# Optimization experiments

Hardware: AMD Instinct MI355X
Metric: run time of the kernel (lower is better)

Reference implementation:

```python
import jax, jax.numpy as jnp
import numpy as np

N, E, D_IN, D_OUT, R, B = 50000, 800000, 100, 100, 200, 50
BN_EPS = 1e-5


def setup_inputs() -> dict:
    key = jax.random.key(0)
    ks = jax.random.split(key, 24)
    inv_in = 1.0 / np.sqrt(D_IN)
    lin = lambda k: (jax.random.uniform(k, (D_OUT, D_IN), jnp.float32, -inv_in, inv_in),
                     jax.random.uniform(jax.random.fold_in(k, 1), (D_OUT,), jnp.float32, -inv_in, inv_in))
    Ws_w, Ws_b = lin(ks[0])
    Wk_w, Wk_b = lin(ks[1])
    Wq_w, Wq_b = lin(ks[2])
    Wv_w, Wv_b = lin(ks[3])
    Wr_w, Wr_b = lin(ks[4])
    return {
        "n_in_feats": jax.random.normal(ks[5], (N, D_IN), jnp.float32),
        "r_feats": jax.random.normal(ks[6], (R, D_IN), jnp.float32),
        "src": jax.random.randint(ks[7], (E,), 0, N),
        "dst": jax.random.randint(ks[8], (E,), 0, N),
        "etype": jax.random.randint(ks[9], (E,), 0, R),
        "norm": jax.random.uniform(ks[10], (E, 1), jnp.float32),
        "Ws_w": Ws_w, "Ws_b": Ws_b,
        "Wk_w": Wk_w, "Wk_b": Wk_b,
        "Wq_w": Wq_w, "Wq_b": Wq_b,
        "Wv_w": Wv_w, "Wv_b": Wv_b,
        "Wr_w": Wr_w, "Wr_b": Wr_b,
        "relation_att": jax.random.normal(ks[11], (B, D_OUT), jnp.float32) * np.sqrt(2.0 / (B + D_OUT)),
        "w_comp": jax.random.normal(ks[12], (R, B), jnp.float32) * np.sqrt(2.0 / (R + B)),
        "alpha": jnp.ones((1,), jnp.float32),
        "loop_rel": jax.random.normal(ks[13], (1, D_IN), jnp.float32) * np.sqrt(2.0 / (1 + D_IN)),
        "bn_gamma": jnp.ones((D_OUT,), jnp.float32),
        "bn_beta": jnp.zeros((D_OUT,), jnp.float32),
    }


def reference(n_in_feats, r_feats, src, dst, etype, norm,
              Ws_w, Ws_b, Wk_w, Wk_b, Wq_w, Wq_b, Wv_w, Wv_b, Wr_w, Wr_b,
              relation_att, w_comp, alpha, loop_rel, bn_gamma, bn_beta):
    num_nodes = n_in_feats.shape[0]
    # relation features incl. self-loop relation (appended row)
    r_all = jnp.concatenate([r_feats, loop_rel], axis=0)          # [R+1, D_in]
    # basis-decomposed per-relation attention weights: [R, D_out]
    rel_w = jnp.matmul(w_comp, relation_att)
    # node projections, then gather per edge (edge_attention)
    k = jnp.matmul(n_in_feats, Wk_w.T) + Wk_b                     # [N, D_out]
    q = jnp.matmul(n_in_feats, Wq_w.T) + Wq_b
    v = jnp.matmul(n_in_feats, Wv_w.T) + Wv_b
    k_e = k[src]                                                   # [E, D_out]
    q_e = q[dst]
    v_e = v[src]
    w_e = rel_w[etype]                                             # [E, D_out]
    att = jnp.sum(k_e * w_e * q_e, axis=-1)                       # [E]
    # segment softmax over incoming edges of each dst node
    seg_max = jax.ops.segment_max(att, dst, num_segments=num_nodes)
    e = jnp.exp(att - seg_max[dst])
    denom = jax.ops.segment_sum(e, dst, num_segments=num_nodes)
    att_w = e / denom[dst]                                         # [E]
    final = jax.ops.segment_sum(att_w[:, None] * v_e, dst, num_segments=num_nodes)  # [N, D_out]
    # gated combination (dropout is identity in eval)
    a = jax.nn.sigmoid(alpha[0])
    n_out = a * (jnp.matmul(n_in_feats, Ws_w.T) + Ws_b) + (1.0 - a) * final
    # BatchNorm1d (training-mode batch stats, biased variance)
    mu = jnp.mean(n_out, axis=0)
    var = jnp.mean((n_out - mu) ** 2, axis=0)
    n_out = (n_out - mu) * jax.lax.rsqrt(var + BN_EPS) * bn_gamma + bn_beta
    n_out = jnp.tanh(n_out)
    r_out = jnp.matmul(r_all, Wr_w.T) + Wr_b                      # [R+1, D_out]
    return n_out, r_out[:-1]
```

## Files before the change

### kernel.cpp

```cpp
#include <hip/hip_runtime.h>
#include <hip/hip_bf16.h>
#include <math.h>

#define N_NODES 50000
#define N_EDGES 800000
#define BN_EPS  1e-5f
#define SCAN_NB 49
#define AGG_NB  2048

typedef float floatx2 __attribute__((ext_vector_type(2)));
typedef _Float16 half2_t __attribute__((ext_vector_type(2)));

#if defined(__has_builtin) && __has_builtin(__builtin_amdgcn_fdot2)
#define FDOT2(a, b, c) __builtin_amdgcn_fdot2((a), (b), (c), false)
#else
#define FDOT2(a, b, c) ((c) + (float)(a).x * (float)(b).x + (float)(a).y * (float)(b).y)
#endif

union h2u { half2_t h; unsigned u; };

#define OFS_RELW   0
#define OFS_KVP    25600
#define OFS_Q      3225600
#define OFS_BNPART 9625600
#define OFS_BNSC   10035200
#define OFS_BNSH   10035328
#define OFS_CNT    10035456
#define OFS_PART   10085632
#define OFS_BSUM   10135808
#define OFS_OFFS   10135872
#define OFS_RANK   10186048
#define OFS_PEDGE  10986048
#define OFS_WT     11786048
#define WS_ELEMS   11806848

__global__ __launch_bounds__(256) void prep_kernel(
    const float* __restrict__ wcomp, const float* __restrict__ ratt,
    const float* __restrict__ Wk, const float* __restrict__ Wq,
    const float* __restrict__ Wv, const float* __restrict__ Ws,
    float* __restrict__ relw, unsigned* __restrict__ Wth,
    int* __restrict__ cnt)
{
    const int b = blockIdx.x;
    const int tid = threadIdx.x;
    if (b < 196) {
        int i = b * 256 + tid;
        if (i < 50176) cnt[i] = 0;
    } else if (b < 296) {
        int o = (b - 196) * 256 + tid;
        if (o < 200 * 128) {
            int r = o / 128, c = o % 128;
            float acc = 0.f;
            if (c < 100) {
                #pragma unroll 10
                for (int k = 0; k < 50; ++k)
                    acc += wcomp[r * 50 + k] * ratt[k * 100 + c];
            }
            relw[o] = acc;
        }
    } else {
        int o = (b - 296) * 256 + tid;
        if (o < 4 * 50 * 104) {
            int m = o / 5200, rem = o % 5200, d2 = rem / 104, c = rem % 104;
            const float* W = (m == 0) ? Wk : (m == 1) ? Wq : (m == 2) ? Wv : Ws;
            float a = (c < 100) ? W[c * 100 + 2 * d2]     : 0.f;
            float bb = (c < 100) ? W[c * 100 + 2 * d2 + 1] : 0.f;
            h2u cv; cv.h = half2_t{(_Float16)a, (_Float16)bb};
            Wth[o] = cv.u;
        }
    }
}

__global__ __launch_bounds__(512) void proj_kernel(
    const float* __restrict__ X, const unsigned* __restrict__ Wth,
    const float* __restrict__ bk, const float* __restrict__ bq,
    const float* __restrict__ bv, const float* __restrict__ bs,
    unsigned* __restrict__ kvp, float* __restrict__ qo,
    float* __restrict__ so)
{
    __shared__ unsigned Xth[50][68];
    __shared__ unsigned Wlh[50][104];
    const int tid = threadIdx.x;
    const int nb  = blockIdx.x * 64;
    const int m   = blockIdx.y;

    const float* bp = (m == 0) ? bk : (m == 1) ? bq : (m == 2) ? bv : bs;

    for (int idx = tid; idx < 1300; idx += 512) {
        int r = idx / 26, c4 = idx % 26;
        uint4 w = ((const uint4*)(Wth + m * 5200 + r * 104))[c4];
        *(uint4*)&Wlh[r][c4 * 4] = w;
    }
    for (int idx = tid; idx < 1600; idx += 512) {
        int n = idx / 25, d4 = idx % 25;
        int node = nb + n;
        float4 x = (node < N_NODES)
                   ? ((const float4*)(X + (size_t)node * 100))[d4]
                   : make_float4(0.f, 0.f, 0.f, 0.f);
        const int col = n ^ ((d4 & 7) << 2);
        h2u c0, c1;
        c0.h = half2_t{(_Float16)x.x, (_Float16)x.y};
        c1.h = half2_t{(_Float16)x.z, (_Float16)x.w};
        Xth[2 * d4][col]     = c0.u;
        Xth[2 * d4 + 1][col] = c1.u;
    }
    __syncthreads();

    const int nt  = tid & 15;
    const int ct  = tid >> 4;
    const bool act = (ct < 25);
    const int cts  = act ? ct : 24;

    float acc[4][4];
    #pragma unroll
    for (int i = 0; i < 4; ++i)
        #pragma unroll
        for (int j = 0; j < 4; ++j) acc[i][j] = 0.f;

    #pragma unroll 5
    for (int d2 = 0; d2 < 50; ++d2) {
        const int key = ((d2 >> 1) & 7) << 2;
        const uint4 xv = *(const uint4*)&Xth[d2][(4 * nt) ^ key];
        const uint4 wv = *(const uint4*)&Wlh[d2][4 * cts];
        h2u x0, x1, x2, x3, w0, w1, w2, w3;
        x0.u = xv.x; x1.u = xv.y; x2.u = xv.z; x3.u = xv.w;
        w0.u = wv.x; w1.u = wv.y; w2.u = wv.z; w3.u = wv.w;
        acc[0][0] = FDOT2(x0.h, w0.h, acc[0][0]);
        acc[0][1] = FDOT2(x0.h, w1.h, acc[0][1]);
        acc[0][2] = FDOT2(x0.h, w2.h, acc[0][2]);
        acc[0][3] = FDOT2(x0.h, w3.h, acc[0][3]);
        acc[1][0] = FDOT2(x1.h, w0.h, acc[1][0]);
        acc[1][1] = FDOT2(x1.h, w1.h, acc[1][1]);
        acc[1][2] = FDOT2(x1.h, w2.h, acc[1][2]);
        acc[1][3] = FDOT2(x1.h, w3.h, acc[1][3]);
        acc[2][0] = FDOT2(x2.h, w0.h, acc[2][0]);
        acc[2][1] = FDOT2(x2.h, w1.h, acc[2][1]);
        acc[2][2] = FDOT2(x2.h, w2.h, acc[2][2]);
        acc[2][3] = FDOT2(x2.h, w3.h, acc[2][3]);
        acc[3][0] = FDOT2(x3.h, w0.h, acc[3][0]);
        acc[3][1] = FDOT2(x3.h, w1.h, acc[3][1]);
        acc[3][2] = FDOT2(x3.h, w2.h, acc[3][2]);
        acc[3][3] = FDOT2(x3.h, w3.h, acc[3][3]);
    }

    const float4 bb = act ? *(const float4*)(bp + ct * 4)
                          : make_float4(0.f, 0.f, 0.f, 0.f);
    if (m == 0 || m == 2) {
        const int wofs = (m == 0) ? ct : (32 + ct);
        #pragma unroll
        for (int i = 0; i < 4; ++i) {
            const int node = nb + nt * 4 + i;
            if (node < N_NODES) {
                unsigned wdo = 0u;
                if (act) {
                    int wd = 0;
                    wd = __builtin_amdgcn_cvt_pk_fp8_f32(
                        acc[i][0] + bb.x, acc[i][1] + bb.y, wd, false);
                    wd = __builtin_amdgcn_cvt_pk_fp8_f32(
                        acc[i][2] + bb.z, acc[i][3] + bb.w, wd, true);
                    wdo = (unsigned)wd;
                }
                kvp[(size_t)node * 64 + wofs] = wdo;
            }
        }
    } else if (m == 1) {
        #pragma unroll
        for (int i = 0; i < 4; ++i) {
            const int node = nb + nt * 4 + i;
            if (node < N_NODES) {
                float4 r = act ? make_float4(acc[i][0] + bb.x, acc[i][1] + bb.y,
                                             acc[i][2] + bb.z, acc[i][3] + bb.w)
                               : make_float4(0.f, 0.f, 0.f, 0.f);
                *(float4*)(qo + (size_t)node * 128 + ct * 4) = r;
            }
        }
    } else {
        if (act) {
            #pragma unroll
            for (int i = 0; i < 4; ++i) {
                const int node = nb + nt * 4 + i;
                if (node < N_NODES) {
                    float4 r = make_float4(acc[i][0] + bb.x, acc[i][1] + bb.y,
                                           acc[i][2] + bb.z, acc[i][3] + bb.w);
                    *(float4*)(so + (size_t)node * 100 + ct * 4) = r;
                }
            }
        }
    }
}

__global__ __launch_bounds__(256) void hist_kernel(
    const int* __restrict__ dst, int* __restrict__ cnt, int* __restrict__ rank)
{
    int e = blockIdx.x * 256 + threadIdx.x;
    if (e < N_EDGES) rank[e] = atomicAdd(&cnt[dst[e]], 1);
}

__global__ __launch_bounds__(1024) void scanA_kernel(
    const int* __restrict__ cnt, int* __restrict__ partial, int* __restrict__ bsum)
{
    __shared__ int buf[1024];
    int tid = threadIdx.x;
    int i = blockIdx.x * 1024 + tid;
    int val = (i < N_NODES) ? cnt[i] : 0;
    buf[tid] = val;
    __syncthreads();
    for (int off = 1; off < 1024; off <<= 1) {
        int t = (tid >= off) ? buf[tid - off] : 0;
        __syncthreads();
        buf[tid] += t;
        __syncthreads();
    }
    int incl = buf[tid];
    if (i < N_NODES) partial[i] = incl - val;
    if (tid == 1023) bsum[blockIdx.x] = incl;
}

__global__ __launch_bounds__(1024) void scanB_kernel(
    const int* __restrict__ partial, const int* __restrict__ bsum,
    int* __restrict__ offs)
{
    __shared__ int bs[64];
    int tid = threadIdx.x;
    if (tid < SCAN_NB) bs[tid] = bsum[tid];
    __syncthreads();
    if (tid == 0) {
        int run = 0;
        for (int b = 0; b < SCAN_NB; ++b) { int t = bs[b]; bs[b] = run; run += t; }
    }
    __syncthreads();
    for (int i = tid; i < N_NODES; i += 1024) offs[i] = partial[i] + bs[i >> 10];
    if (tid == 0) offs[N_NODES] = N_EDGES;
}

__global__ __launch_bounds__(256) void scatter_kernel(
    const int* __restrict__ src, const int* __restrict__ dst,
    const int* __restrict__ ety, const int* __restrict__ offs,
    const int* __restrict__ rank, unsigned* __restrict__ pedge)
{
    int e = blockIdx.x * 256 + threadIdx.x;
    if (e >= N_EDGES) return;
    int d = dst[e];
    pedge[offs[d] + rank[e]] = (unsigned)src[e] | ((unsigned)ety[e] << 17);
}

__global__ __launch_bounds__(256) void agg_kernel(
    const int* __restrict__ offs, const unsigned* __restrict__ pedge,
    const unsigned* __restrict__ kvp, const float* __restrict__ q,
    const float* __restrict__ relw, const float* __restrict__ alpha,
    float* __restrict__ out, float* __restrict__ bnpart)
{
    __shared__ float ls[100], lq[100];
    const int tid = threadIdx.x;
    if (tid < 100) { ls[tid] = 0.f; lq[tid] = 0.f; }
    __syncthreads();
    const int lane = tid & 63;
    const int gwave = blockIdx.x * 4 + (tid >> 6);
    const int nwaves = AGG_NB * 4;
    const float a = 1.f / (1.f + __expf(-alpha[0]));
    const float b = 1.f - a;
    const int cl = lane;
    const bool act = (cl < 50);
    const unsigned short* kv16 = (const unsigned short*)kvp;
    float sx = 0.f, sy = 0.f, qx = 0.f, qy = 0.f;

    for (int n = gwave; n < N_NODES; n += nwaves) {
        const int beg = offs[n], end = offs[n + 1];
        const float2 qv = ((const float2*)(q + (size_t)n * 128))[cl];
        float ax = 0.f, ay = 0.f, wsum = 0.f;
        int i = beg;
        for (; i + 2 <= end; i += 2) {
            const unsigned p0 = pedge[i], p1 = pedge[i + 1];
            const int s0 = (int)(p0 & 0x1FFFFu), t0 = (int)(p0 >> 17);
            const int s1 = (int)(p1 & 0x1FFFFu), t1 = (int)(p1 >> 17);
            const unsigned short* r0 = kv16 + (size_t)s0 * 128;
            const unsigned short* r1 = kv16 + (size_t)s1 * 128;
            const unsigned short kh0 = r0[cl],      kh1 = r1[cl];
            const unsigned short vh0 = r0[64 + cl], vh1 = r1[64 + cl];
            const float2 wv0 = ((const float2*)(relw + t0 * 128))[cl];
            const float2 wv1 = ((const float2*)(relw + t1 * 128))[cl];
            const floatx2 k0 = __builtin_amdgcn_cvt_pk_f32_fp8((int)kh0, false);
            const floatx2 k1 = __builtin_amdgcn_cvt_pk_f32_fp8((int)kh1, false);
            float pa = k0[0] * wv0.x * qv.x + k0[1] * wv0.y * qv.y;
            float pb = k1[0] * wv1.x * qv.x + k1[1] * wv1.y * qv.y;
            #pragma unroll
            for (int off = 32; off > 0; off >>= 1) {
                pa += __shfl_xor(pa, off, 64);
                pb += __shfl_xor(pb, off, 64);
            }
            const float w0 = __expf(pa), w1 = __expf(pb);
            wsum += w0 + w1;
            const floatx2 v0 = __builtin_amdgcn_cvt_pk_f32_fp8((int)vh0, false);
            const floatx2 v1 = __builtin_amdgcn_cvt_pk_f32_fp8((int)vh1, false);
            ax += w0 * v0[0] + w1 * v1[0];
            ay += w0 * v0[1] + w1 * v1[1];
        }
        for (; i < end; ++i) {
            const unsigned p0 = pedge[i];
            const int s0 = (int)(p0 & 0x1FFFFu), t0 = (int)(p0 >> 17);
            const unsigned short* r0 = kv16 + (size_t)s0 * 128;
            const unsigned short kh0 = r0[cl];
            const unsigned short vh0 = r0[64 + cl];
            const float2 wv0 = ((const float2*)(relw + t0 * 128))[cl];
            const floatx2 k0 = __builtin_amdgcn_cvt_pk_f32_fp8((int)kh0, false);
            float pa = k0[0] * wv0.x * qv.x + k0[1] * wv0.y * qv.y;
            #pragma unroll
            for (int off = 32; off > 0; off >>= 1)
                pa += __shfl_xor(pa, off, 64);
            const float w0 = __expf(pa);
            wsum += w0;
            const floatx2 v0 = __builtin_amdgcn_cvt_pk_f32_fp8((int)vh0, false);
            ax += w0 * v0[0];
            ay += w0 * v0[1];
        }
        const float inv = (wsum > 0.f) ? 1.f / wsum : 0.f;
        if (act) {
            float2* po = (float2*)(out + (size_t)n * 100);
            float2 cur = po[cl];
            float v0 = a * cur.x + b * ax * inv;
            float v1 = a * cur.y + b * ay * inv;
            po[cl] = make_float2(v0, v1);
            sx += v0; qx += v0 * v0;
            sy += v1; qy += v1 * v1;
        }
    }
    if (act) {
        atomicAdd(&ls[2 * cl], sx);     atomicAdd(&ls[2 * cl + 1], sy);
        atomicAdd(&lq[2 * cl], qx);     atomicAdd(&lq[2 * cl + 1], qy);
    }
    __syncthreads();
    if (tid < 100) {
        bnpart[(size_t)tid * AGG_NB + blockIdx.x]         = ls[tid];
        bnpart[(size_t)(tid + 100) * AGG_NB + blockIdx.x] = lq[tid];
    }
}

__global__ __launch_bounds__(256) void bnfin_kernel(
    const float* __restrict__ bnpart,
    const float* __restrict__ gamma, const float* __restrict__ beta,
    float* __restrict__ bnsc, float* __restrict__ bnsh)
{
    const int c = blockIdx.x * 4 + (threadIdx.x >> 6);
    const int lane = threadIdx.x & 63;
    if (c >= 100) return;
    float s = 0.f, q = 0.f;
    for (int b2 = lane; b2 < AGG_NB; b2 += 64) {
        s += bnpart[(size_t)c * AGG_NB + b2];
        q += bnpart[(size_t)(c + 100) * AGG_NB + b2];
    }
    #pragma unroll
    for (int off = 32; off > 0; off >>= 1) {
        s += __shfl_xor(s, off, 64);
        q += __shfl_xor(q, off, 64);
    }
    if (lane == 0) {
        const float inv_n = 1.f / (float)N_NODES;
        float mean = s * inv_n;
        float var = q * inv_n - mean * mean;
        float sc = gamma[c] * rsqrtf(var + BN_EPS);
        bnsc[c] = sc;
        bnsh[c] = beta[c] - mean * sc;
    }
}

__global__ __launch_bounds__(256) void applyrout_kernel(
    float* __restrict__ out, const float* __restrict__ bnsc,
    const float* __restrict__ bnsh,
    const float* __restrict__ rf, const float* __restrict__ Wr,
    const float* __restrict__ br)
{
    if (blockIdx.x < 2048) {
        const int total4 = N_NODES * 25;
        for (int idx = blockIdx.x * 256 + threadIdx.x; idx < total4; idx += 2048 * 256) {
            float4* p = ((float4*)out) + idx;
            const int c = (idx % 25) * 4;
            float4 t = *p;
            t.x = tanhf(t.x * bnsc[c]     + bnsh[c]);
            t.y = tanhf(t.y * bnsc[c + 1] + bnsh[c + 1]);
            t.z = tanhf(t.z * bnsc[c + 2] + bnsh[c + 2]);
            t.w = tanhf(t.w * bnsc[c + 3] + bnsh[c + 3]);
            *p = t;
        }
    } else {
        int o = (blockIdx.x - 2048) * 256 + threadIdx.x;
        if (o < 200 * 100) {
            int r = o / 100, c = o % 100;
            float acc = br[c];
            #pragma unroll 10
            for (int d = 0; d < 100; ++d) acc += rf[r * 100 + d] * Wr[c * 100 + d];
            out[N_NODES * 100 + o] = acc;
        }
    }
}

extern "C" void kernel_launch(void* const* d_in, const int* in_sizes, int n_in,
                              void* d_out, int out_size, void* d_ws, size_t ws_size,
                              hipStream_t stream) {
    const float* X     = (const float*)d_in[0];
    const float* rfeat = (const float*)d_in[1];
    const int*   src   = (const int*)d_in[2];
    const int*   dst   = (const int*)d_in[3];
    const int*   ety   = (const int*)d_in[4];
    const float* Wsw   = (const float*)d_in[6];
    const float* Wsb   = (const float*)d_in[7];
    const float* Wkw   = (const float*)d_in[8];
    const float* Wkb   = (const float*)d_in[9];
    const float* Wqw   = (const float*)d_in[10];
    const float* Wqb   = (const float*)d_in[11];
    const float* Wvw   = (const float*)d_in[12];
    const float* Wvb   = (const float*)d_in[13];
    const float* Wrw   = (const float*)d_in[14];
    const float* Wrb   = (const float*)d_in[15];
    const float* ratt  = (const float*)d_in[16];
    const float* wcomp = (const float*)d_in[17];
    const float* alpha = (const float*)d_in[18];
    const float* gamma = (const float*)d_in[20];
    const float* beta  = (const float*)d_in[21];

    float* out = (float*)d_out;
    float* ws  = (float*)d_ws;
    if (ws_size < (size_t)WS_ELEMS * sizeof(float)) return;

    float* relw          = ws + OFS_RELW;
    unsigned* kvp        = (unsigned*)(ws + OFS_KVP);
    float* q             = ws + OFS_Q;
    float* bnpart        = ws + OFS_BNPART;
    float* bnsc          = ws + OFS_BNSC;
    float* bnsh          = ws + OFS_BNSH;
    unsigned* Wth        = (unsigned*)(ws + OFS_WT);
    int* cnt             = (int*)(ws + OFS_CNT);
    int* partial         = (int*)(ws + OFS_PART);
    int* bsum            = (int*)(ws + OFS_BSUM);
    int* offs            = (int*)(ws + OFS_OFFS);
    int* rank            = (int*)(ws + OFS_RANK);
    unsigned* pedge      = (unsigned*)(ws + OFS_PEDGE);

    prep_kernel<<<196 + 100 + 82, 256, 0, stream>>>(
        wcomp, ratt, Wkw, Wqw, Wvw, Wsw, relw, Wth, cnt);
    proj_kernel<<<dim3((N_NODES + 63) / 64, 4), 512, 0, stream>>>(
        X, Wth, Wkb, Wqb, Wvb, Wsb, kvp, q, out);

    hist_kernel<<<(N_EDGES + 255) / 256, 256, 0, stream>>>(dst, cnt, rank);
    scanA_kernel<<<SCAN_NB, 1024, 0, stream>>>(cnt, partial, bsum);
    scanB_kernel<<<1, 1024, 0, stream>>>(partial, bsum, offs);
    scatter_kernel<<<(N_EDGES + 255) / 256, 256, 0, stream>>>(
        src, dst, ety, offs, rank, pedge);

    agg_kernel<<<AGG_NB, 256, 0, stream>>>(
        offs, pedge, kvp, q, relw, alpha, out, bnpart);
    bnfin_kernel<<<25, 256, 0, stream>>>(bnpart, gamma, beta, bnsc, bnsh);
    applyrout_kernel<<<2048 + (20000 + 255) / 256, 256, 0, stream>>>(
        out, bnsc, bnsh, rfeat, Wrw, Wrb);
}
```

Measured before the change: 233.9 us.

## Split wave into four 16-lane groups to score four edges per step

The attention-score phase of the aggregation kernel now lets each 16-lane quarter of a wave handle a different edge. Each lane loads 8 FP8 key values as two 32-bit words plus float4 weights, so the dot-product reduction drops from a 6-step 64-lane shuffle to a 4-step 16-lane one and covers four edges per iteration. The four weights and source ids are then broadcast so the full wave accumulates the value rows as before. This removes the separate pair and tail loops and cuts shuffle latency per edge, at the cost of extra broadcast shuffles and lanes left idle when a node's degree is not a multiple of four.

After: 228.9 us. 1.02x faster.

```diff
diff --git a/kernel.cpp b/kernel.cpp
--- a/kernel.cpp
+++ b/kernel.cpp
@@ -255,78 +255,74 @@
     if (tid < 100) { ls[tid] = 0.f; lq[tid] = 0.f; }
     __syncthreads();
     const int lane = tid & 63;
+    const int j    = lane & 15;
+    const int g16  = lane >> 4;
     const int gwave = blockIdx.x * 4 + (tid >> 6);
     const int nwaves = AGG_NB * 4;
     const float a = 1.f / (1.f + __expf(-alpha[0]));
     const float b = 1.f - a;
-    const int cl = lane;
-    const bool act = (cl < 50);
+    const bool act = (lane < 50);
     const unsigned short* kv16 = (const unsigned short*)kvp;
     float sx = 0.f, sy = 0.f, qx = 0.f, qy = 0.f;
 
     for (int n = gwave; n < N_NODES; n += nwaves) {
         const int beg = offs[n], end = offs[n + 1];
-        const float2 qv = ((const float2*)(q + (size_t)n * 128))[cl];
+        const float4 qa = ((const float4*)(q + (size_t)n * 128))[j];
+        const float4 qb = ((const float4*)(q + (size_t)n * 128))[j + 16];
         float ax = 0.f, ay = 0.f, wsum = 0.f;
-        int i = beg;
-        for (; i + 2 <= end; i += 2) {
-            const unsigned p0 = pedge[i], p1 = pedge[i + 1];
-            const int s0 = (int)(p0 & 0x1FFFFu), t0 = (int)(p0 >> 17);
-            const int s1 = (int)(p1 & 0x1FFFFu), t1 = (int)(p1 >> 17);
-            const unsigned short* r0 = kv16 + (size_t)s0 * 128;
-            const unsigned short* r1 = kv16 + (size_t)s1 * 128;
-            const unsigned short kh0 = r0[cl],      kh1 = r1[cl];
-            const unsigned short vh0 = r0[64 + cl], vh1 = r1[64 + cl];
-            const float2 wv0 = ((const float2*)(relw + t0 * 128))[cl];
-            const float2 wv1 = ((const float2*)(relw + t1 * 128))[cl];
-            const floatx2 k0 = __builtin_amdgcn_cvt_pk_f32_fp8((int)kh0, false);
-            const floatx2 k1 = __builtin_amdgcn_cvt_pk_f32_fp8((int)kh1, false);
-            float pa = k0[0] * wv0.x * qv.x + k0[1] * wv0.y * qv.y;
-            float pb = k1[0] * wv1.x * qv.x + k1[1] * wv1.y * qv.y;
+        for (int i = beg; i < end; i += 4) {
+            const int ne = end - i;
+            const int gg = (g16 < ne) ? g16 : (ne - 1);
+            const unsigned pw = pedge[i + gg];
+            const int s_ = (int)(pw & 0x1FFFFu);
+            const int t_ = (int)(pw >> 17);
+            const unsigned* kr = kvp + (size_t)s_ * 64;
+            const unsigned kh0 = kr[j];
+            const unsigned kh1 = kr[j + 16];
+            const float4 w0 = ((const float4*)(relw + t_ * 128))[j];
+            const float4 w1 = ((const float4*)(relw + t_ * 128))[j + 16];
+            const floatx2 ka = __builtin_amdgcn_cvt_pk_f32_fp8((int)kh0, false);
+            const floatx2 kb = __builtin_amdgcn_cvt_pk_f32_fp8((int)kh0, true);
+            const floatx2 kc = __builtin_amdgcn_cvt_pk_f32_fp8((int)kh1, false);
+            const floatx2 kd = __builtin_amdgcn_cvt_pk_f32_fp8((int)kh1, true);
+            float pa = ka[0] * w0.x * qa.x + ka[1] * w0.y * qa.y
+                     + kb[0] * w0.z * qa.z + kb[1] * w0.w * qa.w
+                     + kc[0] * w1.x * qb.x + kc[1] * w1.y * qb.y
+                     + kd[0] * w1.z * qb.z + kd[1] * w1.w * qb.w;
             #pragma unroll
-            for (int off = 32; off > 0; off >>= 1) {
-                pa += __shfl_xor(pa, off, 64);
-                pb += __shfl_xor(pb, off, 64);
-            }
-            const float w0 = __expf(pa), w1 = __expf(pb);
-            wsum += w0 + w1;
-            const floatx2 v0 = __builtin_amdgcn_cvt_pk_f32_fp8((int)vh0, false);
-            const floatx2 v1 = __builtin_amdgcn_cvt_pk_f32_fp8((int)vh1, false);
-            ax += w0 * v0[0] + w1 * v1[0];
-            ay += w0 * v0[1] + w1 * v1[1];
-        }
-        for (; i < end; ++i) {
-            const unsigned p0 = pedge[i];
-            const int s0 = (int)(p0 & 0x1FFFFu), t0 = (int)(p0 >> 17);
-            const unsigned short* r0 = kv16 + (size_t)s0 * 128;
-            const unsigned short kh0 = r0[cl];
-            const unsigned short vh0 = r0[64 + cl];
-            const float2 wv0 = ((const float2*)(relw + t0 * 128))[cl];
-            const floatx2 k0 = __builtin_amdgcn_cvt_pk_f32_fp8((int)kh0, false);
-            float pa = k0[0] * wv0.x * qv.x + k0[1] * wv0.y * qv.y;
-            #pragma unroll
-            for (int off = 32; off > 0; off >>= 1)
-                pa += __shfl_xor(pa, off, 64);
-            const float w0 = __expf(pa);
-            wsum += w0;
-            const floatx2 v0 = __builtin_amdgcn_cvt_pk_f32_fp8((int)vh0, false);
-            ax += w0 * v0[0];
-            ay += w0 * v0[1];
+            for (int off = 1; off < 16; off <<= 1)
+                pa += __shfl_xor(pa, off, 16);
+            const float wgt = (g16 < ne) ? __expf(pa) : 0.f;
+            const float wA = __shfl(wgt, 0, 64),  wB = __shfl(wgt, 16, 64);
+            const float wC = __shfl(wgt, 32, 64), wD = __shfl(wgt, 48, 64);
+            const int   sA = __shfl(s_, 0, 64),   sB = __shfl(s_, 16, 64);
+            const int   sC = __shfl(s_, 32, 64),  sD = __shfl(s_, 48, 64);
+            wsum += wA + wB + wC + wD;
+            const unsigned short vA = kv16[(size_t)sA * 128 + 64 + lane];
+            const unsigned short vB = kv16[(size_t)sB * 128 + 64 + lane];
+            const unsigned short vC = kv16[(size_t)sC * 128 + 64 + lane];
+            const unsigned short vD = kv16[(size_t)sD * 128 + 64 + lane];
+            const floatx2 fA = __builtin_amdgcn_cvt_pk_f32_fp8((int)vA, false);
+            const floatx2 fB = __builtin_amdgcn_cvt_pk_f32_fp8((int)vB, false);
+            const floatx2 fC = __builtin_amdgcn_cvt_pk_f32_fp8((int)vC, false);
+            const floatx2 fD = __builtin_amdgcn_cvt_pk_f32_fp8((int)vD, false);
+            ax += wA * fA[0] + wB * fB[0] + wC * fC[0] + wD * fD[0];
+            ay += wA * fA[1] + wB * fB[1] + wC * fC[1] + wD * fD[1];
         }
         const float inv = (wsum > 0.f) ? 1.f / wsum : 0.f;
         if (act) {
             float2* po = (float2*)(out + (size_t)n * 100);
-            float2 cur = po[cl];
+            float2 cur = po[lane];
             float v0 = a * cur.x + b * ax * inv;
             float v1 = a * cur.y + b * ay * inv;
-            po[cl] = make_float2(v0, v1);
+            po[lane] = make_float2(v0, v1);
             sx += v0; qx += v0 * v0;
             sy += v1; qy += v1 * v1;
         }
     }
     if (act) {
-        atomicAdd(&ls[2 * cl], sx);     atomicAdd(&ls[2 * cl + 1], sy);
-        atomicAdd(&lq[2 * cl], qx);     atomicAdd(&lq[2 * cl + 1], qy);
+        atomicAdd(&ls[2 * lane], sx);     atomicAdd(&ls[2 * lane + 1], sy);
+        atomicAdd(&lq[2 * lane], qx);     atomicAdd(&lq[2 * lane + 1], qy);
     }
     __syncthreads();
     if (tid < 100) {
```
